# Kernel optimization log

Hardware: AMD Instinct MI355X
Metric: run time of the kernel (lower is better)

The kernel has to match this reference:

```python
import jax, jax.numpy as jnp
import numpy as np

MODE_STATIC = 0
MODE_APPEARANCE_CHANGE = 2
MODE_BLINK = 3
MODE_AFFINE = 4


def _affine_warp(src, theta):
    """F.affine_grid + F.grid_sample(bilinear, zeros, align_corners=False).

    src:   [N, C, H, W]
    theta: [N, 2, 3]
    """
    N, C, H, W = src.shape
    dt = src.dtype
    # affine_grid base coords (align_corners=False): centers of pixels in [-1, 1]
    xs = (jnp.arange(W, dtype=dt) * 2 + 1) / W - 1  # [W]
    ys = (jnp.arange(H, dtype=dt) * 2 + 1) / H - 1  # [H]
    gx = (theta[:, 0, 0][:, None, None] * xs[None, None, :]
          + theta[:, 0, 1][:, None, None] * ys[None, :, None]
          + theta[:, 0, 2][:, None, None])  # [N, H, W]
    gy = (theta[:, 1, 0][:, None, None] * xs[None, None, :]
          + theta[:, 1, 1][:, None, None] * ys[None, :, None]
          + theta[:, 1, 2][:, None, None])  # [N, H, W]
    # unnormalize (align_corners=False)
    ix = ((gx + 1) * W - 1) / 2
    iy = ((gy + 1) * H - 1) / 2
    x0 = jnp.floor(ix)
    y0 = jnp.floor(iy)
    wx1 = ix - x0
    wy1 = iy - y0
    wx0 = 1 - wx1
    wy0 = 1 - wy1
    x0i = x0.astype(jnp.int32)
    y0i = y0.astype(jnp.int32)

    src_flat = src.reshape(N, C, H * W)

    def gather(xi, yi):
        valid = (xi >= 0) & (xi < W) & (yi >= 0) & (yi < H)  # zeros padding
        xi_c = jnp.clip(xi, 0, W - 1)
        yi_c = jnp.clip(yi, 0, H - 1)
        idx = (yi_c * W + xi_c).reshape(N, 1, H * W)
        v = jnp.take_along_axis(src_flat, idx, axis=2).reshape(N, C, H, W)
        return v * valid.astype(dt)[:, None]

    out = (gather(x0i, y0i) * (wx0 * wy0)[:, None]
           + gather(x0i + 1, y0i) * (wx1 * wy0)[:, None]
           + gather(x0i, y0i + 1) * (wx0 * wy1)[:, None]
           + gather(x0i + 1, y0i + 1) * (wx1 * wy1)[:, None])
    return out


def setup_inputs() -> dict:
    key = jax.random.key(0)
    ks = jax.random.split(key, 7)
    B, NI, C, H, W = 4, 16, 3, 256, 256
    g0 = jax.random.normal(ks[0], (B, NI, C, H, W), dtype=jnp.float32)
    m0 = jax.random.uniform(ks[1], (B, NI, 1, H, W), dtype=jnp.float32)
    mode_logits = jax.random.normal(ks[2], (B, NI, 5), dtype=jnp.float32)
    # near-identity affine transforms (realistic small motions)
    ident = jnp.array([1.0, 0.0, 0.0, 0.0, 1.0, 0.0], dtype=jnp.float32)
    transform_params = ident + 0.1 * jax.random.normal(ks[3], (B, NI, 6), dtype=jnp.float32)
    alpha = jax.random.uniform(ks[4], (B, NI, 1), dtype=jnp.float32)
    instance_valid = (jax.random.uniform(ks[5], (B, NI)) > 0.2).astype(jnp.float32)
    i_bg = jax.random.normal(ks[6], (B, C, H, W), dtype=jnp.float32)
    return {"g0": g0, "m0": m0, "mode_logits": mode_logits,
            "transform_params": transform_params, "alpha": alpha,
            "instance_valid": instance_valid, "i_bg": i_bg}


def reference(g0, m0, mode_logits, transform_params, alpha, instance_valid, i_bg):
    B, NI, C, H, W = g0.shape
    theta = transform_params.reshape(-1, 2, 3)  # [B*NI, 2, 3]
    warped_overlay = _affine_warp(g0.reshape(B * NI, C, H, W), theta).reshape(B, NI, C, H, W)
    warped_mask = _affine_warp(m0.reshape(B * NI, 1, H, W), theta).reshape(B, NI, 1, H, W)

    mode_ids = jnp.argmax(mode_logits, axis=-1)  # [B, NI]
    static_like = ((mode_ids == MODE_STATIC) | (mode_ids == MODE_APPEARANCE_CHANGE)
                   | (mode_ids == MODE_AFFINE)).astype(g0.dtype)[:, :, None, None, None]
    blink = (mode_ids == MODE_BLINK).astype(g0.dtype)[:, :, None, None, None]
    alpha_map = alpha[:, :, :, None, None]  # [B, NI, 1, 1, 1]
    valid = instance_valid[:, :, None, None, None]

    g_mid_per_instance = (static_like * warped_overlay + blink * warped_overlay * alpha_map) * valid
    m_mid_per_instance = (static_like * warped_mask + blink * warped_mask * alpha_map) * valid
    g_mid = g_mid_per_instance.sum(axis=1)
    m_mid = jnp.clip(m_mid_per_instance.sum(axis=1), 0.0, 1.0)
    i_base = i_bg + g_mid
    return (g_mid_per_instance, m_mid_per_instance, g_mid, m_mid, i_base)
```

## Files before the change

kernel.cpp:

```cpp
#include <hip/hip_runtime.h>

#define BB 4
#define NI 16
#define CC 3
#define HH 256
#define WW 256
#define HWSZ (HH * WW)

typedef float f2v __attribute__((ext_vector_type(2)));
typedef f2v f2u __attribute__((aligned(4)));

__device__ __forceinline__ f2v ld2(const float* __restrict__ p) {
    return *reinterpret_cast<const f2u*>(p);
}

__device__ __forceinline__ float inst_params(
    const float* __restrict__ ml, const float* __restrict__ tp,
    const float* __restrict__ al, const float* __restrict__ iv,
    int id, float th[6]) {
    float best = ml[id * 5];
    int bid = 0;
#pragma unroll
    for (int k = 1; k < 5; ++k) {
        float v = ml[id * 5 + k];
        if (v > best) { best = v; bid = k; }
    }
    float coef = (bid == 0 || bid == 2 || bid == 4) ? 1.0f
               : (bid == 3 ? al[id] : 0.0f);
    coef *= iv[id];
#pragma unroll
    for (int k = 0; k < 6; ++k) th[k] = tp[id * 6 + k];
    return coef;
}

struct Samp {
    int oA, oB;
    float wxA, wxB;
    float wyA, wyB;
};

__device__ __forceinline__ Samp make_samp(const float th[6], float coef, int p) {
    const int h = p >> 8, w = p & (WW - 1);
    const float xs = (2 * w + 1) * (1.0f / WW) - 1.0f;
    const float ys = (2 * h + 1) * (1.0f / HH) - 1.0f;
    const float gx = th[0] * xs + th[1] * ys + th[2];
    const float gy = th[3] * xs + th[4] * ys + th[5];
    const float ix = gx * (0.5f * WW) + (0.5f * WW - 0.5f);
    const float iy = gy * (0.5f * HH) + (0.5f * HH - 0.5f);
    const float x0f = floorf(ix), y0f = floorf(iy);
    const float wx1 = ix - x0f, wy1 = iy - y0f;
    const float wx0 = 1.0f - wx1, wy0 = 1.0f - wy1;
    const int x0 = (int)x0f, y0 = (int)y0f;
    const int x1 = x0 + 1, y1 = y0 + 1;
    const float wx0v = ((unsigned)x0 < (unsigned)WW) ? wx0 : 0.0f;
    const float wx1v = ((unsigned)x1 < (unsigned)WW) ? wx1 : 0.0f;
    const float wy0v = ((unsigned)y0 < (unsigned)HH) ? (coef * wy0) : 0.0f;
    const float wy1v = ((unsigned)y1 < (unsigned)HH) ? (coef * wy1) : 0.0f;
    const int bx = min(max(x0, 0), WW - 2);
    const int by = min(max(y0, 0), HH - 2);
    const bool sx = (x0 != bx);
    const bool sy = (y0 != by);
    Samp s;
    s.wxA = sx ? wx1v : wx0v;  s.wxB = sx ? wx0v : wx1v;
    s.wyA = sy ? wy1v : wy0v;  s.wyB = sy ? wy0v : wy1v;
    s.oA = by * WW + bx;
    s.oB = s.oA + WW;
    return s;
}

__device__ __forceinline__ float bilerp(const float* __restrict__ src, const Samp& s) {
    const f2v a = ld2(src + s.oA);
    const f2v b = ld2(src + s.oB);
    return s.wyA * (s.wxA * a.x + s.wxB * a.y)
         + s.wyB * (s.wxA * b.x + s.wxB * b.y);
}

__global__ __launch_bounds__(512) void fused_k(
    const float* __restrict__ g0,
    const float* __restrict__ m0,
    const float* __restrict__ ml,
    const float* __restrict__ tp,
    const float* __restrict__ al,
    const float* __restrict__ iv,
    const float* __restrict__ i_bg,
    float* __restrict__ out_gpi,
    float* __restrict__ out_mpi,
    float* __restrict__ out_gmid,
    float* __restrict__ out_mmid,
    float* __restrict__ out_ibase) {
    const int f     = blockIdx.x;
    const int slot  = f & 7;
    const int b     = slot >> 1;
    const int yhalf = slot & 1;
    const int zz    = (f >> 3) & 1;
    const int patch = f >> 4;
    const int row   = threadIdx.x >> 6;
    const int col   = threadIdx.x & 63;
    const int px0   = (patch & 3) * 64;
    const int py0   = yhalf * 128 + (patch >> 2) * 8;
    const int p     = (py0 + row) * WW + px0 + col;

    const size_t offA = zz ? (size_t)(2 * HWSZ) : 0;

    float sA = 0.f, sB = 0.f;

#pragma unroll 2
    for (int ii = 0; ii < NI; ++ii) {
        const int id = b * NI + ii;
        float th[6];
        const float coef = inst_params(ml, tp, al, iv, id, th);

        float vA = 0.f, vB = 0.f;
        if (coef != 0.0f) {
            const Samp s = make_samp(th, coef, p);
            const float* gsrc = g0 + (size_t)id * CC * HWSZ;
            const float* srcA = gsrc + offA;
            const float* srcB = zz ? (m0 + (size_t)id * HWSZ) : (gsrc + HWSZ);
            vA = bilerp(srcA, s);
            vB = bilerp(srcB, s);
        }

        float* gp = out_gpi + (size_t)id * CC * HWSZ + p;
        float* dstA = gp + offA;
        float* dstB = zz ? (out_mpi + (size_t)id * HWSZ + p) : (gp + HWSZ);
        __builtin_nontemporal_store(vA, dstA);
        __builtin_nontemporal_store(vB, dstB);

        sA += vA; sB += vB;
    }

    const size_t ob = (size_t)b * CC * HWSZ + p;
    if (zz == 0) {
        out_gmid[ob]            = sA;
        out_gmid[ob + HWSZ]     = sB;
        out_ibase[ob]           = sA + i_bg[ob];
        out_ibase[ob + HWSZ]    = sB + i_bg[ob + HWSZ];
    } else {
        out_gmid[ob + 2 * HWSZ]  = sA;
        out_ibase[ob + 2 * HWSZ] = sA + i_bg[ob + 2 * HWSZ];
        out_mmid[(size_t)b * HWSZ + p] = fminf(fmaxf(sB, 0.f), 1.f);
    }
}

extern "C" void kernel_launch(void* const* d_in, const int* in_sizes, int n_in,
                              void* d_out, int out_size, void* d_ws, size_t ws_size,
                              hipStream_t stream) {
    const float* g0          = (const float*)d_in[0];
    const float* m0          = (const float*)d_in[1];
    const float* mode_logits = (const float*)d_in[2];
    const float* tp          = (const float*)d_in[3];
    const float* alpha       = (const float*)d_in[4];
    const float* iv          = (const float*)d_in[5];
    const float* i_bg        = (const float*)d_in[6];

    float* out       = (float*)d_out;
    float* out_gpi   = out;
    float* out_mpi   = out_gpi  + (size_t)BB * NI * CC * HWSZ;
    float* out_gmid  = out_mpi  + (size_t)BB * NI * HWSZ;
    float* out_mmid  = out_gmid + (size_t)BB * CC * HWSZ;
    float* out_ibase = out_mmid + (size_t)BB * HWSZ;

    fused_k<<<dim3(1024), 512, 0, stream>>>(g0, m0, mode_logits, tp, alpha, iv,
                                            i_bg, out_gpi, out_mpi,
                                            out_gmid, out_mmid, out_ibase);
}
```

Baseline: 154.9 us.

## Stage warped source footprint into shared memory before bilinear sampling

For each instance, the kernel computes the bounding box of source coordinates for the block's 8x64 output patch from its four corners, loads that footprint cooperatively into LDS tiles, and samples the 2x2 neighbourhoods from LDS instead of global memory. When the footprint exceeds the tile size it falls back to direct global loads. The aim is to replace scattered, unaligned global gathers with coalesced loads plus LDS reads. In exchange it adds two __syncthreads per instance, drops the loop unroll, and uses about 28KB of LDS per block, which may lower occupancy and limit latency overlap.

```diff
diff --git a/kernel.cpp b/kernel.cpp
--- a/kernel.cpp
+++ b/kernel.cpp
@@ -6,6 +6,9 @@
 #define HH 256
 #define WW 256
 #define HWSZ (HH * WW)
+
+#define TROWS 26
+#define TSTR  134
 
 typedef float f2v __attribute__((ext_vector_type(2)));
 typedef f2v f2u __attribute__((aligned(4)));
@@ -34,7 +37,7 @@
 }
 
 struct Samp {
-    int oA, oB;
+    int bx, by;
     float wxA, wxB;
     float wyA, wyB;
 };
@@ -63,14 +66,11 @@
     Samp s;
     s.wxA = sx ? wx1v : wx0v;  s.wxB = sx ? wx0v : wx1v;
     s.wyA = sy ? wy1v : wy0v;  s.wyB = sy ? wy0v : wy1v;
-    s.oA = by * WW + bx;
-    s.oB = s.oA + WW;
+    s.bx = bx; s.by = by;
     return s;
 }
 
-__device__ __forceinline__ float bilerp(const float* __restrict__ src, const Samp& s) {
-    const f2v a = ld2(src + s.oA);
-    const f2v b = ld2(src + s.oB);
+__device__ __forceinline__ float lerp22(const f2v a, const f2v b, const Samp& s) {
     return s.wyA * (s.wxA * a.x + s.wxB * a.y)
          + s.wyB * (s.wxA * b.x + s.wxB * b.y);
 }
@@ -88,23 +88,31 @@
     float* __restrict__ out_gmid,
     float* __restrict__ out_mmid,
     float* __restrict__ out_ibase) {
+    __shared__ float tileA[TROWS * TSTR];
+    __shared__ float tileB[TROWS * TSTR];
+
     const int f     = blockIdx.x;
     const int slot  = f & 7;
     const int b     = slot >> 1;
     const int yhalf = slot & 1;
     const int zz    = (f >> 3) & 1;
     const int patch = f >> 4;
-    const int row   = threadIdx.x >> 6;
-    const int col   = threadIdx.x & 63;
+    const int wv    = threadIdx.x >> 6;
+    const int ln    = threadIdx.x & 63;
     const int px0   = (patch & 3) * 64;
     const int py0   = yhalf * 128 + (patch >> 2) * 8;
-    const int p     = (py0 + row) * WW + px0 + col;
+    const int p     = (py0 + wv) * WW + px0 + ln;
 
     const size_t offA = zz ? (size_t)(2 * HWSZ) : 0;
 
+    const float xsL = (2 * px0 + 1) * (1.0f / WW) - 1.0f;
+    const float xsR = (2 * (px0 + 63) + 1) * (1.0f / WW) - 1.0f;
+    const float ysT = (2 * py0 + 1) * (1.0f / HH) - 1.0f;
+    const float ysB = (2 * (py0 + 7) + 1) * (1.0f / HH) - 1.0f;
+
     float sA = 0.f, sB = 0.f;
 
-#pragma unroll 2
+#pragma unroll 1
     for (int ii = 0; ii < NI; ++ii) {
         const int id = b * NI + ii;
         float th[6];
@@ -113,11 +121,54 @@
         float vA = 0.f, vB = 0.f;
         if (coef != 0.0f) {
             const Samp s = make_samp(th, coef, p);
-            const float* gsrc = g0 + (size_t)id * CC * HWSZ;
-            const float* srcA = gsrc + offA;
-            const float* srcB = zz ? (m0 + (size_t)id * HWSZ) : (gsrc + HWSZ);
-            vA = bilerp(srcA, s);
-            vB = bilerp(srcB, s);
+            const float* gsrcA = g0 + (size_t)id * CC * HWSZ + offA;
+            const float* gsrcB = zz ? (m0 + (size_t)id * HWSZ)
+                                    : (g0 + (size_t)id * CC * HWSZ + HWSZ);
+
+            const float ixTL = (th[0] * xsL + th[1] * ysT + th[2]) * (0.5f * WW) + (0.5f * WW - 0.5f);
+            const float ixTR = (th[0] * xsR + th[1] * ysT + th[2]) * (0.5f * WW) + (0.5f * WW - 0.5f);
+            const float ixBL = (th[0] * xsL + th[1] * ysB + th[2]) * (0.5f * WW) + (0.5f * WW - 0.5f);
+            const float ixBR = (th[0] * xsR + th[1] * ysB + th[2]) * (0.5f * WW) + (0.5f * WW - 0.5f);
+            const float iyTL = (th[3] * xsL + th[4] * ysT + th[5]) * (0.5f * HH) + (0.5f * HH - 0.5f);
+            const float iyTR = (th[3] * xsR + th[4] * ysT + th[5]) * (0.5f * HH) + (0.5f * HH - 0.5f);
+            const float iyBL = (th[3] * xsL + th[4] * ysB + th[5]) * (0.5f * HH) + (0.5f * HH - 0.5f);
+            const float iyBR = (th[3] * xsR + th[4] * ysB + th[5]) * (0.5f * HH) + (0.5f * HH - 0.5f);
+            const int x0mn = (int)floorf(fminf(fminf(ixTL, ixTR), fminf(ixBL, ixBR)));
+            const int x0mx = (int)floorf(fmaxf(fmaxf(ixTL, ixTR), fmaxf(ixBL, ixBR)));
+            const int y0mn = (int)floorf(fminf(fminf(iyTL, iyTR), fminf(iyBL, iyBR)));
+            const int y0mx = (int)floorf(fmaxf(fmaxf(iyTL, iyTR), fmaxf(iyBL, iyBR)));
+            const int bxmn = min(max(x0mn, 0), WW - 2);
+            const int bxmx = min(max(x0mx, 0), WW - 2);
+            const int bymn = min(max(y0mn, 0), HH - 2);
+            const int bymx = min(max(y0mx, 0), HH - 2);
+            const int c0    = bxmn & ~1;
+            const int wlen  = bxmx + 2 - c0;
+            const int r0    = bymn;
+            const int nrows = bymx + 2 - r0;
+
+            if (nrows <= TROWS && wlen <= 128) {
+                __syncthreads();
+                for (int r = wv; r < nrows; r += 8) {
+                    const int gr = r0 + r;
+                    const int c  = c0 + 2 * ln;
+                    if (c <= WW - 2) {
+                        const f2v a = ld2(gsrcA + gr * WW + c);
+                        const f2v q = ld2(gsrcB + gr * WW + c);
+                        *(f2u*)&tileA[r * TSTR + 2 * ln] = a;
+                        *(f2u*)&tileB[r * TSTR + 2 * ln] = q;
+                    }
+                }
+                __syncthreads();
+                const int li = (s.by - r0) * TSTR + (s.bx - c0);
+                vA = lerp22(*(const f2u*)&tileA[li],
+                            *(const f2u*)&tileA[li + TSTR], s);
+                vB = lerp22(*(const f2u*)&tileB[li],
+                            *(const f2u*)&tileB[li + TSTR], s);
+            } else {
+                const int oA = s.by * WW + s.bx, oB = oA + WW;
+                vA = lerp22(ld2(gsrcA + oA), ld2(gsrcA + oB), s);
+                vB = lerp22(ld2(gsrcB + oA), ld2(gsrcB + oB), s);
+            }
         }
 
         float* gp = out_gpi + (size_t)id * CC * HWSZ + p;
```

After: 156.4 us. No clear change (+0.9%).
